# Optimization experiments

Measured on AMD Instinct MI355X. Metric: run time of the kernel, lower is better.

## Reference

```python
import jax, jax.numpy as jnp
import numpy as np

SIGMA = 1.0   # noise std (unit-variance synthetic input)
P = 11        # patch size p1
K = 16        # number of similar patches k1
WIN = 65      # search window w (odd)
S = 3         # reference-patch stride
ALPHA = 0.5   # n2n alpha


def _unfold(x, ksize, stride):
    # (N,1,H,W) -> (N, ksize*ksize, Ho, Wo); kernel positions row-major (== torch F.unfold for C=1)
    return jax.lax.conv_general_dilated_patches(
        x, (ksize, ksize), (stride, stride), 'VALID',
        dimension_numbers=('NCHW', 'OIHW', 'NCHW'))


def block_matching(x, k, p, w, s):
    N, _, H, W = x.shape
    v = w // 2
    assert (H - p + 1) % s == 1 and (W - p + 1) % s == 1  # no edge-case branches needed
    Href = (H - p) // s + 1
    Wref = (W - p) // s + 1
    x_pad = jnp.pad(x, ((0, 0), (0, 0), (v, v), (v, v)))  # zero pad; invalid candidates masked below
    # |patch|^2 / p^2 at every position of the padded image (== F.avg_pool2d(x**2, p))
    sq = jax.lax.reduce_window(x_pad * x_pad, 0.0, jax.lax.add,
                               (1, 1, p, p), (1, 1, 1, 1), 'VALID') / (p * p)
    norms = _unfold(sq, 2 * v + 1, s)                                  # (N,(2v+1)^2,Href,Wref)
    norms = norms.reshape(N, 2 * v + 1, 2 * v + 1, Href, Wref).transpose(0, 3, 4, 1, 2)
    lw = _unfold(x_pad, 2 * v + p, s) / p                              # (N,(2v+p)^2,Href,Wref)
    lw = lw.reshape(N, 2 * v + p, 2 * v + p, Href, Wref).transpose(0, 3, 4, 1, 2)
    G = N * Href * Wref
    lw = lw.reshape(1, G, 2 * v + p, 2 * v + p)
    ref = lw[0, :, v:-v, v:-v][:, None]                                # (G,1,p,p) reference patches
    sp = jax.lax.conv_general_dilated(
        lw, ref, (1, 1), 'VALID',
        dimension_numbers=('NCHW', 'OIHW', 'NCHW'),
        feature_group_count=G)                                         # (1,G,2v+1,2v+1)
    dist = norms.reshape(1, G, 2 * v + 1, 2 * v + 1) - 2.0 * sp
    dist = dist.reshape(N, Href, Wref, 2 * v + 1, 2 * v + 1)
    # mask candidate patches that fall outside the original image (torch uses NaN padding + topk)
    offs = jnp.arange(-v, v + 1)
    hr = jnp.arange(Href) * s
    wr = jnp.arange(Wref) * s
    row_ok = (hr[:, None] + offs >= 0) & (hr[:, None] + offs <= H - p)  # (Href, 2v+1)
    col_ok = (wr[:, None] + offs >= 0) & (wr[:, None] + offs <= W - p)  # (Wref, 2v+1)
    valid = row_ok[:, None, :, None] & col_ok[None, :, None, :]
    dist = jnp.where(valid[None], dist, jnp.inf)
    dist = dist.at[..., v, v].set(-jnp.inf)                            # reference patch always kept
    dist = dist.reshape(N, Href, Wref, (2 * v + 1) ** 2)
    _, idx = jax.lax.top_k(-dist, k)                                   # k smallest distances
    ind_row = idx // (2 * v + 1) - v
    ind_col = idx % (2 * v + 1) - v
    ind = (ind_row + hr[None, :, None, None]) * (W - p + 1) + (ind_col + wr[None, None, :, None])
    return ind.reshape(N, -1)                                          # (N, Href*Wref*k)


def gather_groups(y, indices, k, p):
    N = y.shape[0]
    uf = _unfold(y, p, 1).reshape(N, p * p, -1)                        # (N, n, (H-p+1)(W-p+1))
    Yg = jnp.take_along_axis(uf, indices[:, None, :], axis=2)          # (N, n, L*k)
    L = indices.shape[1] // k
    return Yg.reshape(N, p * p, L, k).transpose(0, 2, 3, 1)            # (N, L, k, n)


def denoise1(Y, sigma):
    # method='n2n', constraints='affine'
    N, B, k, n = Y.shape
    D = n * sigma ** 2
    E = n * ALPHA ** 2 * sigma ** 2
    Ik = jnp.eye(k, dtype=Y.dtype)
    Q = Y @ jnp.swapaxes(Y, 2, 3) + E * Ik                             # (N,B,k,k), SPD
    Lc = jnp.linalg.cholesky(Q)
    Ikb = jnp.broadcast_to(Ik, Q.shape)
    Z = jax.scipy.linalg.solve_triangular(Lc, Ikb, lower=True)
    Qinv = jax.scipy.linalg.solve_triangular(jnp.swapaxes(Lc, 2, 3), Z, lower=False)
    Qinv1 = jnp.sum(Qinv, axis=3, keepdims=True)
    Qinv2 = jnp.sum(Qinv1, axis=2, keepdims=True)
    theta = Ik - (Qinv - (Qinv1 @ jnp.swapaxes(Qinv1, 2, 3)) / Qinv2) * (D + E)
    theta = jnp.swapaxes(theta, 2, 3)
    X_hat = theta @ Y
    weights = 1.0 / jnp.clip(jnp.sum(theta * theta, axis=3, keepdims=True), 1.0 / k, 1.0)
    return X_hat, weights


def _fold(x, H, W, p):
    # inverse of unfold: sum overlapping p x p patches back onto the image grid
    N, n, _ = x.shape
    Hp, Wp = H - p + 1, W - p + 1
    x = x.reshape(N, p, p, Hp, Wp)
    out = jnp.zeros((N, 1, H, W), x.dtype)
    for a in range(p):
        for b in range(p):
            out = out.at[:, 0, a:a + Hp, b:b + Wp].add(x[:, a, b])
    return out


def aggregate(X_hat, weights, indices, H, W, p):
    N, L, k, n = X_hat.shape
    X = (X_hat * weights).reshape(N, L * k, n).transpose(0, 2, 1)      # (N, n, L*k)
    Wt = jnp.broadcast_to(weights, (N, L, k, n)).reshape(N, L * k, n).transpose(0, 2, 1)
    Lfull = (H - p + 1) * (W - p + 1)
    def scat(vals, idx):
        return jnp.zeros((n, Lfull), vals.dtype).at[:, idx].add(vals)
    X_sum = jax.vmap(scat)(X, indices)
    W_sum = jax.vmap(scat)(Wt, indices)
    return _fold(X_sum, H, W, p) / _fold(W_sum, H, W, p)


def _forward(y):
    N, C, H, W = y.shape
    indices = block_matching(y, K, P, WIN, S)
    Yg = gather_groups(y, indices, K, P)
    X_hat, weights = denoise1(Yg, SIGMA)
    return aggregate(X_hat, weights, indices, H, W, P)


def setup_inputs():
    key = jax.random.key(0)
    y = jax.random.normal(key, (4, 1, 128, 128), dtype=jnp.float32)
    return {"y": y}


def reference(y):
    return _forward(y)
```

## Files before the change

kernel.cpp:

```cpp
#include <hip/hip_runtime.h>
#include <math.h>

#define HH 128
#define WW 128
#define NIMG 4
#define PP 11
#define KSIM 16
#define STRIDE_S 3
#define VRAD 32
#define WINW 65
#define NTASK (WINW*9)
#define HREF 40
#define WREF 40
#define NPOS 118
#define WROWS 75
#define WPITCH 84
#define NGROUP (NIMG*HREF*WREF)
#define EPS_E 30.25f
#define DE_C 151.25f
#define INFD 3.0e38f
#define RTASK (VRAD*9 + VRAD/8)

#define FOOT 84
#define FPITCH 85
#define SPITCH 88

__global__ __launch_bounds__(256, 5)
void bm_kernel(const float* __restrict__ y, int* __restrict__ inds)
{
    __shared__ float win[WROWS][WPITCH];
    __shared__ float candv[4][16];
    __shared__ int   candi[4][16];

    const int blk = blockIdx.x;
    const int n   = blk / (HREF*WREF);
    const int rem = blk % (HREF*WREF);
    const int hr  = (rem / WREF) * STRIDE_S;
    const int wr  = (rem % WREF) * STRIDE_S;
    const float* img = y + n * HH * WW;
    const int tid = threadIdx.x;

    for (int t = tid; t < WROWS * WPITCH; t += 256) {
        int r = t / WPITCH, c = t % WPITCH;
        int gr = hr - VRAD + r, gc = wr - VRAD + c;
        float v = 0.f;
        if (c < WROWS && gr >= 0 && gr < HH && gc >= 0 && gc < WW)
            v = img[gr * WW + gc];
        win[r][c] = v;
    }
    __syncthreads();

    float d[3][8];
#pragma unroll
    for (int s = 0; s < 3; s++)
#pragma unroll
        for (int c = 0; c < 8; c++) d[s][c] = INFD;

#pragma unroll
    for (int s = 0; s < 3; s++) {
        int task = tid + (s << 8);
        if (task < NTASK) {
            int drx = task / 9;
            int c0  = (task % 9) * 8;
            int rr  = hr + drx - VRAD;
            bool rowok = (rr >= 0 && rr <= HH - PP);
            if (rowok) {
                float dot[8];
                float colsq[18];
#pragma unroll
                for (int c = 0; c < 8; c++) dot[c] = 0.f;
#pragma unroll
                for (int j2 = 0; j2 < 18; j2++) colsq[j2] = 0.f;
                for (int a = 0; a < PP; a++) {
                    const float4* w4 = reinterpret_cast<const float4*>(&win[drx + a][c0]);
                    float4 A0 = w4[0], A1 = w4[1], A2 = w4[2], A3 = w4[3];
                    float2 A4 = *reinterpret_cast<const float2*>(&win[drx + a][c0 + 16]);
                    float wv[18] = {A0.x,A0.y,A0.z,A0.w, A1.x,A1.y,A1.z,A1.w,
                                    A2.x,A2.y,A2.z,A2.w, A3.x,A3.y,A3.z,A3.w,
                                    A4.x,A4.y};
                    const float4* r4 = reinterpret_cast<const float4*>(&win[VRAD + a][VRAD]);
                    float4 R0 = r4[0], R1 = r4[1];
                    float2 R2 = *reinterpret_cast<const float2*>(&win[VRAD + a][VRAD + 8]);
                    float  R3 = win[VRAD + a][VRAD + 10];
                    float rv[11] = {R0.x,R0.y,R0.z,R0.w, R1.x,R1.y,R1.z,R1.w,
                                    R2.x,R2.y, R3};
#pragma unroll
                    for (int j2 = 0; j2 < 18; j2++) colsq[j2] += wv[j2] * wv[j2];
#pragma unroll
                    for (int b = 0; b < PP; b++) {
#pragma unroll
                        for (int c = 0; c < 8; c++)
                            dot[c] += wv[b + c] * rv[b];
                    }
                }
#pragma unroll
                for (int j2 = 1; j2 < 18; j2++) colsq[j2] += colsq[j2 - 1];
#pragma unroll
                for (int c = 0; c < 8; c++) {
                    int dcx = c0 + c;
                    int cc  = wr + dcx - VRAD;
                    float norm = colsq[c + 10] - (c ? colsq[c - 1] : 0.f);
                    if (dcx < WINW && cc >= 0 && cc <= WW - PP)
                        d[s][c] = norm - 2.f * dot[c];
                }
            }
            if (task == RTASK) d[s][0] = -INFD;
        }
    }

    float lval = INFD; int lidx = 0;
#pragma unroll
    for (int s = 0; s < 3; s++)
#pragma unroll
        for (int c = 0; c < 8; c++)
            if (d[s][c] < lval) { lval = d[s][c]; lidx = (s << 3) | c; }

    const int wvid = tid >> 6, lane = tid & 63;
    for (int sel = 0; sel < KSIM; sel++) {
        float rv = lval;
        int   ri = ((tid + ((lidx >> 3) << 8)) << 3) | (lidx & 7);
#pragma unroll
        for (int off = 32; off > 0; off >>= 1) {
            float ov = __shfl_down(rv, off);
            int   oi = __shfl_down(ri, off);
            if (ov < rv) { rv = ov; ri = oi; }
        }
        if (lane == 0) { candv[wvid][sel] = rv; candi[wvid][sel] = ri; }
        int bi = __shfl(ri, 0);
        int otid = (bi >> 3) & 255;
        if (tid == otid) {
            int code = (((bi >> 3) >> 8) << 3) | (bi & 7);
            lval = INFD; lidx = 0;
#pragma unroll
            for (int s = 0; s < 3; s++)
#pragma unroll
                for (int c = 0; c < 8; c++) {
                    if (((s << 3) | c) == code) d[s][c] = INFD;
                    if (d[s][c] < lval) { lval = d[s][c]; lidx = (s << 3) | c; }
                }
        }
    }
    __syncthreads();

    if (wvid == 0) {
        float v  = candv[lane >> 4][lane & 15];
        int   ci = candi[lane >> 4][lane & 15];
        for (int sel = 0; sel < KSIM; sel++) {
            float rv = v; int ri = ci; int rl = lane;
#pragma unroll
            for (int off = 32; off > 0; off >>= 1) {
                float ov = __shfl_down(rv, off);
                int   oi = __shfl_down(ri, off);
                int   ol = __shfl_down(rl, off);
                if (ov < rv) { rv = ov; ri = oi; rl = ol; }
            }
            int bi = __shfl(ri, 0);
            int bl = __shfl(rl, 0);
            if (lane == 0) {
                int task2 = bi >> 3;
                int drx = task2 / 9, dcx = (task2 % 9) * 8 + (bi & 7);
                inds[blk * KSIM + sel] =
                    (hr + drx - VRAD) * NPOS + (wr + dcx - VRAD);
            }
            if (lane == bl) v = INFD;
        }
    }
}

__global__ __launch_bounds__(512, 1)
void dn_kernel(const float* __restrict__ y, const int* __restrict__ inds,
               float2* __restrict__ nd, int R)
{
    __shared__ float  src[FOOT][SPITCH];
    __shared__ float2 acc[FOOT][FPITCH];
    __shared__ float  Qm[16][16][17];
    __shared__ float  s1[16][16];
    __shared__ float  s2[16];
    __shared__ float  wl[16][16];
    __shared__ short  pr_[16][16], pc_[16][16];

    const int blk = blockIdx.x;
    const int n  = blk / 100;
    const int tr = blk % 100;
    const int ti = tr / 10, tj = tr % 10;
    const int r0 = 12*ti - VRAD, c0 = 12*tj - VRAD;
    const int tid = threadIdx.x;
    const float* img = y + n * HH * WW;

    if (tid < 256) {
        int g = tid >> 4, m = tid & 15;
        int gg = n*(HREF*WREF) + (ti*4 + (g >> 2))*WREF + (tj*4 + (g & 3));
        int idx = inds[gg*KSIM + m];
        pr_[g][m] = (short)(idx / NPOS);
        pc_[g][m] = (short)(idx % NPOS);
    }
    for (int t = tid; t < FOOT*FOOT; t += 512) {
        int rr = t / FOOT, cc = t % FOOT;
        int gr = r0 + rr, gc = c0 + cc;
        float v = 0.f;
        if (gr >= 0 && gr < HH && gc >= 0 && gc < WW) v = img[gr*WW + gc];
        src[rr][cc] = v;
    }
    for (int t = tid; t < FOOT*FPITCH; t += 512)
        acc[t/FPITCH][t%FPITCH] = make_float2(0.f, 0.f);
    __syncthreads();

    for (int k = 0; k < 5; k++) {
        int task = tid + k*512;
        if (task < 16*136) {
            int g = task / 136, e = task % 136;
            int i = (int)((sqrtf(8.f*(float)e + 1.f) - 1.f) * 0.5f + 1e-4f);
            int j = e - i*(i+1)/2;
            int ari = pr_[g][i] - r0, aci = pc_[g][i] - c0;
            int arj = pr_[g][j] - r0, acj = pc_[g][j] - c0;
            float s = (i == j) ? EPS_E : 0.f;
            for (int a = 0; a < PP; a++) {
                const float* Ri = &src[ari + a][aci];
                const float* Rj = &src[arj + a][acj];
#pragma unroll
                for (int b = 0; b < PP; b++) s += Ri[b] * Rj[b];
            }
            Qm[g][i][j] = s;
            Qm[g][j][i] = s;
        }
    }
    __syncthreads();

    const int uu = tid >> 8, ii = (tid >> 4) & 15, jj = tid & 15;
    for (int ks = 0; ks < 16; ks++) {
        float fA[8], rk[8], pv[8], aij[8];
#pragma unroll
        for (int k = 0; k < 8; k++) {
            int g = uu + 2*k;
            fA[k]  = Qm[g][ii][ks];
            rk[k]  = Qm[g][ks][jj];
            pv[k]  = Qm[g][ks][ks];
            aij[k] = Qm[g][ii][jj];
        }
        __syncthreads();
#pragma unroll
        for (int k = 0; k < 8; k++) {
            int g = uu + 2*k;
            float inv = 1.f / pv[k];
            float nv;
            if (ii == ks) nv = (jj == ks) ? inv : rk[k] * inv;
            else          nv = (jj == ks) ? -fA[k] * inv : aij[k] - fA[k] * rk[k] * inv;
            Qm[g][ii][jj] = nv;
        }
        __syncthreads();
    }

    if (tid < 256) {
        int g = tid >> 4, a = tid & 15;
        float s = 0.f;
#pragma unroll
        for (int b = 0; b < 16; b++) s += Qm[g][a][b];
        s1[g][a] = s;
    }
    __syncthreads();
    if (tid < 16) {
        float s = 0.f;
#pragma unroll
        for (int a = 0; a < 16; a++) s += s1[tid][a];
        s2[tid] = s;
    }
    __syncthreads();
#pragma unroll
    for (int k = 0; k < 8; k++) {
        int g = uu + 2*k;
        float t = ((ii == jj) ? 1.f : 0.f)
                - (Qm[g][ii][jj] - s1[g][ii]*s1[g][jj]/s2[g]) * DE_C;
        Qm[g][ii][jj] = t;
    }
    __syncthreads();
    if (tid < 256) {
        int g = tid >> 4, r = tid & 15;
        float s = 0.f;
#pragma unroll
        for (int m2 = 0; m2 < 16; m2++) { float t = Qm[g][m2][r]; s += t*t; }
        s = fminf(fmaxf(s, 1.f/16.f), 1.f);
        wl[g][r] = 1.f / s;
    }
    __syncthreads();

    for (int it = 0; it < 2; it++) {
        int task = tid + it*512;
        if (task < 16*61) {
            int g = task / 61, s = task % 61;
            int pxa = 2*s;
            bool okB = (pxa + 1 < 121);
            int dra = pxa / 11, dca = pxa % 11;
            int drb = dra, dcb = dca + 1;
            if (dcb == 11) { drb = dra + 1; dcb = 0; }
            if (!okB) { drb = dra; dcb = dca; }

            int baseS[16];
#pragma unroll
            for (int m = 0; m < 16; m++)
                baseS[m] = ((int)pr_[g][m] - r0) * SPITCH + ((int)pc_[g][m] - c0);

            const float* sf = &src[0][0];
            float xhA[16], xhB[16];
#pragma unroll
            for (int r = 0; r < 16; r++) { xhA[r] = 0.f; xhB[r] = 0.f; }
            const int offA = dra*SPITCH + dca, offB = drb*SPITCH + dcb;
#pragma unroll
            for (int m = 0; m < 16; m++) {
                float yvA = sf[baseS[m] + offA];
                float yvB = sf[baseS[m] + offB];
#pragma unroll
                for (int r = 0; r < 16; r++) {
                    float t = Qm[g][m][r];
                    xhA[r] += t * yvA;
                    xhB[r] += t * yvB;
                }
            }
#pragma unroll
            for (int r = 0; r < 16; r++) {
                float wv2 = wl[g][r];
                int ar = (int)pr_[g][r] - r0, ac = (int)pc_[g][r] - c0;
                float* cA = (float*)&acc[ar + dra][ac + dca];
                __hip_atomic_fetch_add(cA,     wv2 * xhA[r],
                    __ATOMIC_RELAXED, __HIP_MEMORY_SCOPE_WORKGROUP);
                __hip_atomic_fetch_add(cA + 1, wv2,
                    __ATOMIC_RELAXED, __HIP_MEMORY_SCOPE_WORKGROUP);
                if (okB) {
                    float* cB = (float*)&acc[ar + drb][ac + dcb];
                    __hip_atomic_fetch_add(cB,     wv2 * xhB[r],
                        __ATOMIC_RELAXED, __HIP_MEMORY_SCOPE_WORKGROUP);
                    __hip_atomic_fetch_add(cB + 1, wv2,
                        __ATOMIC_RELAXED, __HIP_MEMORY_SCOPE_WORKGROUP);
                }
            }
        }
    }
    __syncthreads();

    float2* ndI = nd + ((size_t)(blk & (R - 1)) * NIMG + n) * HH * WW;
    for (int t = tid; t < FOOT * FOOT; t += 512) {
        int rr = t / FOOT, cc = t % FOOT;
        float2 v = acc[rr][cc];
        if (v.y != 0.f) {
            int px = (r0 + rr) * WW + (c0 + cc);
#if defined(__has_builtin) && __has_builtin(__builtin_amdgcn_global_atomic_fadd_v2f32)
            typedef float v2f __attribute__((ext_vector_type(2)));
            __builtin_amdgcn_global_atomic_fadd_v2f32((v2f*)&ndI[px], (v2f){v.x, v.y});
#else
            atomicAdd(&ndI[px].x, v.x);
            atomicAdd(&ndI[px].y, v.y);
#endif
        }
    }
}

__global__ __launch_bounds__(256)
void fin_kernel(const float2* __restrict__ nd, float* __restrict__ out, int R)
{
    int t = blockIdx.x * 256 + threadIdx.x;
    if (t < NIMG * HH * WW) {
        float sn = 0.f, sd = 0.f;
        for (int r = 0; r < R; r++) {
            float2 v = nd[(size_t)r * NIMG * HH * WW + t];
            sn += v.x; sd += v.y;
        }
        out[t] = sn / sd;
    }
}

extern "C" void kernel_launch(void* const* d_in, const int* in_sizes, int n_in,
                              void* d_out, int out_size, void* d_ws, size_t ws_size,
                              hipStream_t stream)
{
    const float* y = (const float*)d_in[0];
    float* out = (float*)d_out;

    size_t indsBytes = (size_t)NGROUP * KSIM * sizeof(int);
    size_t perRep    = (size_t)NIMG * HH * WW * sizeof(float2);
    int R = 1;
    while (R < 4 && indsBytes + perRep * (size_t)(R * 2) <= ws_size) R <<= 1;

    float2* nd  = (float2*)d_ws;
    int*    inds = (int*)((char*)d_ws + perRep * (size_t)R);

    hipMemsetAsync(nd, 0, perRep * (size_t)R, stream);
    bm_kernel<<<NGROUP, 256, 0, stream>>>(y, inds);
    dn_kernel<<<NIMG * 100, 512, 0, stream>>>(y, inds, nd, R);
    fin_kernel<<<(NIMG * HH * WW + 255) / 256, 256, 0, stream>>>(nd, out, R);
}
```

Measured before the change: 504.3 us.

## Tile block matching over 4x4 reference groups with shared row-dot reuse

Block matching moves from one workgroup per reference patch to one workgroup per 4x4 tile of reference patches. Each tile computes 11-wide row dot products in shared memory once, and those partial sums are reused across the overlapping references. Patch norms are precomputed by a new kernel, and each reference keeps a per-lane sorted top-16 list, merged across 16 lanes with xor shuffles. The denoise kernel's shared accumulator is split into two halves to cut LDS use and raise occupancy, at the cost of a second pass with extra syncs.

```diff
diff --git a/kernel.cpp b/kernel.cpp
--- a/kernel.cpp
+++ b/kernel.cpp
@@ -9,170 +9,173 @@
 #define STRIDE_S 3
 #define VRAD 32
 #define WINW 65
-#define NTASK (WINW*9)
 #define HREF 40
 #define WREF 40
 #define NPOS 118
-#define WROWS 75
-#define WPITCH 84
 #define NGROUP (NIMG*HREF*WREF)
 #define EPS_E 30.25f
 #define DE_C 151.25f
 #define INFD 3.0e38f
-#define RTASK (VRAD*9 + VRAD/8)
 
 #define FOOT 84
 #define FPITCH 85
 #define SPITCH 88
-
-__global__ __launch_bounds__(256, 5)
-void bm_kernel(const float* __restrict__ y, int* __restrict__ inds)
+#define IPITCH 100
+#define PD2 388
+#define DBATCH 96
+#define PADW 72
+#define PADDD (WINW*PADW)
+#define NBATCH 49
+#define CNP 120
+
+__global__ __launch_bounds__(128)
+void bm_norm(const float* __restrict__ y, float* __restrict__ cnorm)
 {
-    __shared__ float win[WROWS][WPITCH];
-    __shared__ float candv[4][16];
-    __shared__ int   candi[4][16];
+    int n = blockIdx.x / NPOS, rr = blockIdx.x % NPOS;
+    int cc = threadIdx.x;
+    if (cc < NPOS) {
+        const float* img = y + n * HH * WW;
+        float s = 0.f;
+        for (int a = 0; a < PP; a++) {
+            const float* rp = &img[(rr + a) * WW + cc];
+#pragma unroll
+            for (int b = 0; b < PP; b++) s += rp[b] * rp[b];
+        }
+        cnorm[n * NPOS * CNP + rr * CNP + cc] = s;
+    }
+}
+
+__global__ __launch_bounds__(256, 2)
+void bm_kernel(const float* __restrict__ y, const float* __restrict__ cnorm,
+               int* __restrict__ inds)
+{
+    __shared__ float timg[FOOT][IPITCH];
+    __shared__ float D2[20][PD2];
 
     const int blk = blockIdx.x;
-    const int n   = blk / (HREF*WREF);
-    const int rem = blk % (HREF*WREF);
-    const int hr  = (rem / WREF) * STRIDE_S;
-    const int wr  = (rem % WREF) * STRIDE_S;
+    const int n  = blk / 100;
+    const int tr = blk % 100;
+    const int ti = tr / 10, tj = tr % 10;
+    const int r0 = 12 * ti - VRAD, c0 = 12 * tj - VRAD;
+    const int tid = threadIdx.x;
     const float* img = y + n * HH * WW;
-    const int tid = threadIdx.x;
-
-    for (int t = tid; t < WROWS * WPITCH; t += 256) {
-        int r = t / WPITCH, c = t % WPITCH;
-        int gr = hr - VRAD + r, gc = wr - VRAD + c;
+    const float* cn  = cnorm + n * NPOS * CNP;
+
+    for (int t = tid; t < FOOT * IPITCH; t += 256) {
+        int r = t / IPITCH, c = t % IPITCH;
+        int gr = r0 + r, gc = c0 + c;
         float v = 0.f;
-        if (c < WROWS && gr >= 0 && gr < HH && gc >= 0 && gc < WW)
+        if (c < FOOT && gr >= 0 && gr < HH && gc >= 0 && gc < WW)
             v = img[gr * WW + gc];
-        win[r][c] = v;
-    }
-    __syncthreads();
-
-    float d[3][8];
-#pragma unroll
-    for (int s = 0; s < 3; s++)
-#pragma unroll
-        for (int c = 0; c < 8; c++) d[s][c] = INFD;
-
-#pragma unroll
-    for (int s = 0; s < 3; s++) {
-        int task = tid + (s << 8);
-        if (task < NTASK) {
-            int drx = task / 9;
-            int c0  = (task % 9) * 8;
-            int rr  = hr + drx - VRAD;
-            bool rowok = (rr >= 0 && rr <= HH - PP);
-            if (rowok) {
-                float dot[8];
-                float colsq[18];
-#pragma unroll
-                for (int c = 0; c < 8; c++) dot[c] = 0.f;
-#pragma unroll
-                for (int j2 = 0; j2 < 18; j2++) colsq[j2] = 0.f;
-                for (int a = 0; a < PP; a++) {
-                    const float4* w4 = reinterpret_cast<const float4*>(&win[drx + a][c0]);
-                    float4 A0 = w4[0], A1 = w4[1], A2 = w4[2], A3 = w4[3];
-                    float2 A4 = *reinterpret_cast<const float2*>(&win[drx + a][c0 + 16]);
-                    float wv[18] = {A0.x,A0.y,A0.z,A0.w, A1.x,A1.y,A1.z,A1.w,
-                                    A2.x,A2.y,A2.z,A2.w, A3.x,A3.y,A3.z,A3.w,
-                                    A4.x,A4.y};
-                    const float4* r4 = reinterpret_cast<const float4*>(&win[VRAD + a][VRAD]);
-                    float4 R0 = r4[0], R1 = r4[1];
-                    float2 R2 = *reinterpret_cast<const float2*>(&win[VRAD + a][VRAD + 8]);
-                    float  R3 = win[VRAD + a][VRAD + 10];
-                    float rv[11] = {R0.x,R0.y,R0.z,R0.w, R1.x,R1.y,R1.z,R1.w,
-                                    R2.x,R2.y, R3};
-#pragma unroll
-                    for (int j2 = 0; j2 < 18; j2++) colsq[j2] += wv[j2] * wv[j2];
-#pragma unroll
-                    for (int b = 0; b < PP; b++) {
-#pragma unroll
-                        for (int c = 0; c < 8; c++)
-                            dot[c] += wv[b + c] * rv[b];
+        timg[r][c] = v;
+    }
+    __syncthreads();
+
+    float sv[16]; int si[16];
+#pragma unroll
+    for (int q = 0; q < 16; q++) { sv[q] = INFD; si[q] = 0; }
+
+    const int prow1 = tid / 12;
+    const int dcc   = tid % 12;
+    const int refq  = tid >> 4;
+    const int dl    = tid & 15;
+    const int u = refq >> 2, v = refq & 3;
+    const int hr = 3 * (4 * ti + u), wr = 3 * (4 * tj + v);
+
+#pragma unroll 1
+    for (int b = 0; b < NBATCH; b++) {
+        if (tid < 240) {
+            int ddp0 = b * DBATCH + dcc * 8;
+            if (ddp0 < PADDD) {
+                int dr   = ddp0 / PADW - VRAD;
+                int dcx0 = ddp0 % PADW;
+                const float* row1 = &timg[(VRAD + prow1)][VRAD];
+                const float* row2 = &timg[(VRAD + prow1 + dr)][dcx0];
+                float a1[20], a2[27];
+#pragma unroll
+                for (int q = 0; q < 5; q++) {
+                    float4 x4 = ((const float4*)row1)[q];
+                    a1[4*q] = x4.x; a1[4*q+1] = x4.y; a1[4*q+2] = x4.z; a1[4*q+3] = x4.w;
+                }
+#pragma unroll
+                for (int q = 0; q < 27; q++) a2[q] = row2[q];
+#pragma unroll
+                for (int k = 0; k < 8; k++) {
+                    float d0 = 0.f, d1 = 0.f, d2 = 0.f, d3 = 0.f;
+#pragma unroll
+                    for (int bb = 0; bb < PP; bb++) {
+                        d0 += a1[bb]     * a2[bb + k];
+                        d1 += a1[3 + bb] * a2[3 + bb + k];
+                        d2 += a1[6 + bb] * a2[6 + bb + k];
+                        d3 += a1[9 + bb] * a2[9 + bb + k];
+                    }
+                    *(float4*)&D2[prow1][(dcc * 8 + k) * 4] = make_float4(d0, d1, d2, d3);
+                }
+            }
+        }
+        __syncthreads();
+#pragma unroll
+        for (int kk = 0; kk < 6; kk++) {
+            int d = dl + 16 * kk;
+            int ddp = b * DBATCH + d;
+            if (ddp < PADDD) {
+                int dcx = ddp % PADW;
+                if (dcx < WINW) {
+                    int dr = ddp / PADW - VRAD, dc = dcx - VRAD;
+                    int rr = hr + dr, cc = wr + dc;
+                    if (rr >= 0 && rr <= HH - PP && cc >= 0 && cc <= WW - PP) {
+                        float dot = 0.f;
+#pragma unroll
+                        for (int a = 0; a < PP; a++)
+                            dot += D2[3 * u + a][d * 4 + v];
+                        float val = cn[rr * CNP + cc] - 2.f * dot;
+                        if (dr == 0 && dc == 0) val = -INFD;
+                        if (val < sv[15]) {
+                            sv[15] = val; si[15] = ddp;
+#pragma unroll
+                            for (int q = 15; q > 0; q--) {
+                                if (sv[q] < sv[q - 1]) {
+                                    float tv = sv[q]; sv[q] = sv[q-1]; sv[q-1] = tv;
+                                    int   tq = si[q]; si[q] = si[q-1]; si[q-1] = tq;
+                                }
+                            }
+                        }
                     }
                 }
-#pragma unroll
-                for (int j2 = 1; j2 < 18; j2++) colsq[j2] += colsq[j2 - 1];
-#pragma unroll
-                for (int c = 0; c < 8; c++) {
-                    int dcx = c0 + c;
-                    int cc  = wr + dcx - VRAD;
-                    float norm = colsq[c + 10] - (c ? colsq[c - 1] : 0.f);
-                    if (dcx < WINW && cc >= 0 && cc <= WW - PP)
-                        d[s][c] = norm - 2.f * dot[c];
-                }
             }
-            if (task == RTASK) d[s][0] = -INFD;
-        }
-    }
-
-    float lval = INFD; int lidx = 0;
-#pragma unroll
-    for (int s = 0; s < 3; s++)
-#pragma unroll
-        for (int c = 0; c < 8; c++)
-            if (d[s][c] < lval) { lval = d[s][c]; lidx = (s << 3) | c; }
-
-    const int wvid = tid >> 6, lane = tid & 63;
+        }
+        __syncthreads();
+    }
+
+    const int gref = n * (HREF * WREF) + (ti * 4 + u) * WREF + (tj * 4 + v);
+#pragma unroll 1
     for (int sel = 0; sel < KSIM; sel++) {
-        float rv = lval;
-        int   ri = ((tid + ((lidx >> 3) << 8)) << 3) | (lidx & 7);
-#pragma unroll
-        for (int off = 32; off > 0; off >>= 1) {
-            float ov = __shfl_down(rv, off);
-            int   oi = __shfl_down(ri, off);
-            if (ov < rv) { rv = ov; ri = oi; }
-        }
-        if (lane == 0) { candv[wvid][sel] = rv; candi[wvid][sel] = ri; }
-        int bi = __shfl(ri, 0);
-        int otid = (bi >> 3) & 255;
-        if (tid == otid) {
-            int code = (((bi >> 3) >> 8) << 3) | (bi & 7);
-            lval = INFD; lidx = 0;
-#pragma unroll
-            for (int s = 0; s < 3; s++)
-#pragma unroll
-                for (int c = 0; c < 8; c++) {
-                    if (((s << 3) | c) == code) d[s][c] = INFD;
-                    if (d[s][c] < lval) { lval = d[s][c]; lidx = (s << 3) | c; }
-                }
-        }
-    }
-    __syncthreads();
-
-    if (wvid == 0) {
-        float v  = candv[lane >> 4][lane & 15];
-        int   ci = candi[lane >> 4][lane & 15];
-        for (int sel = 0; sel < KSIM; sel++) {
-            float rv = v; int ri = ci; int rl = lane;
-#pragma unroll
-            for (int off = 32; off > 0; off >>= 1) {
-                float ov = __shfl_down(rv, off);
-                int   oi = __shfl_down(ri, off);
-                int   ol = __shfl_down(rl, off);
-                if (ov < rv) { rv = ov; ri = oi; rl = ol; }
-            }
-            int bi = __shfl(ri, 0);
-            int bl = __shfl(rl, 0);
-            if (lane == 0) {
-                int task2 = bi >> 3;
-                int drx = task2 / 9, dcx = (task2 % 9) * 8 + (bi & 7);
-                inds[blk * KSIM + sel] =
-                    (hr + drx - VRAD) * NPOS + (wr + dcx - VRAD);
-            }
-            if (lane == bl) v = INFD;
+        float bv = sv[0]; int bi = si[0]; int bl = dl;
+#pragma unroll
+        for (int m = 1; m < 16; m <<= 1) {
+            float ov = __shfl_xor(bv, m, 16);
+            int   oi = __shfl_xor(bi, m, 16);
+            int   ol = __shfl_xor(bl, m, 16);
+            if (ov < bv || (ov == bv && ol < bl)) { bv = ov; bi = oi; bl = ol; }
+        }
+        if (dl == 0) {
+            int dr = bi / PADW - VRAD, dc = bi % PADW - VRAD;
+            inds[gref * KSIM + sel] = (hr + dr) * NPOS + (wr + dc);
+        }
+        if (dl == bl) {
+#pragma unroll
+            for (int q = 0; q < 15; q++) { sv[q] = sv[q + 1]; si[q] = si[q + 1]; }
+            sv[15] = INFD;
         }
     }
 }
 
-__global__ __launch_bounds__(512, 1)
+__global__ __launch_bounds__(512, 4)
 void dn_kernel(const float* __restrict__ y, const int* __restrict__ inds,
                float2* __restrict__ nd, int R)
 {
     __shared__ float  src[FOOT][SPITCH];
-    __shared__ float2 acc[FOOT][FPITCH];
+    __shared__ float2 accH[42][FPITCH];
     __shared__ float  Qm[16][16][17];
     __shared__ float  s1[16][16];
     __shared__ float  s2[16];
@@ -183,34 +186,32 @@
     const int n  = blk / 100;
     const int tr = blk % 100;
     const int ti = tr / 10, tj = tr % 10;
-    const int r0 = 12*ti - VRAD, c0 = 12*tj - VRAD;
+    const int r0 = 12 * ti - VRAD, c0 = 12 * tj - VRAD;
     const int tid = threadIdx.x;
     const float* img = y + n * HH * WW;
 
     if (tid < 256) {
         int g = tid >> 4, m = tid & 15;
-        int gg = n*(HREF*WREF) + (ti*4 + (g >> 2))*WREF + (tj*4 + (g & 3));
-        int idx = inds[gg*KSIM + m];
+        int gg = n * (HREF * WREF) + (ti * 4 + (g >> 2)) * WREF + (tj * 4 + (g & 3));
+        int idx = inds[gg * KSIM + m];
         pr_[g][m] = (short)(idx / NPOS);
         pc_[g][m] = (short)(idx % NPOS);
     }
-    for (int t = tid; t < FOOT*FOOT; t += 512) {
+    for (int t = tid; t < FOOT * FOOT; t += 512) {
         int rr = t / FOOT, cc = t % FOOT;
         int gr = r0 + rr, gc = c0 + cc;
-        float v = 0.f;
-        if (gr >= 0 && gr < HH && gc >= 0 && gc < WW) v = img[gr*WW + gc];
-        src[rr][cc] = v;
-    }
-    for (int t = tid; t < FOOT*FPITCH; t += 512)
-        acc[t/FPITCH][t%FPITCH] = make_float2(0.f, 0.f);
+        float vv = 0.f;
+        if (gr >= 0 && gr < HH && gc >= 0 && gc < WW) vv = img[gr * WW + gc];
+        src[rr][cc] = vv;
+    }
     __syncthreads();
 
     for (int k = 0; k < 5; k++) {
-        int task = tid + k*512;
-        if (task < 16*136) {
+        int task = tid + k * 512;
+        if (task < 16 * 136) {
             int g = task / 136, e = task % 136;
-            int i = (int)((sqrtf(8.f*(float)e + 1.f) - 1.f) * 0.5f + 1e-4f);
-            int j = e - i*(i+1)/2;
+            int i = (int)((sqrtf(8.f * (float)e + 1.f) - 1.f) * 0.5f + 1e-4f);
+            int j = e - i * (i + 1) / 2;
             int ari = pr_[g][i] - r0, aci = pc_[g][i] - c0;
             int arj = pr_[g][j] - r0, acj = pc_[g][j] - c0;
             float s = (i == j) ? EPS_E : 0.f;
@@ -231,7 +232,7 @@
         float fA[8], rk[8], pv[8], aij[8];
 #pragma unroll
         for (int k = 0; k < 8; k++) {
-            int g = uu + 2*k;
+            int g = uu + 2 * k;
             fA[k]  = Qm[g][ii][ks];
             rk[k]  = Qm[g][ks][jj];
             pv[k]  = Qm[g][ks][ks];
@@ -240,7 +241,7 @@
         __syncthreads();
 #pragma unroll
         for (int k = 0; k < 8; k++) {
-            int g = uu + 2*k;
+            int g = uu + 2 * k;
             float inv = 1.f / pv[k];
             float nv;
             if (ii == ks) nv = (jj == ks) ? inv : rk[k] * inv;
@@ -254,7 +255,7 @@
         int g = tid >> 4, a = tid & 15;
         float s = 0.f;
 #pragma unroll
-        for (int b = 0; b < 16; b++) s += Qm[g][a][b];
+        for (int b2 = 0; b2 < 16; b2++) s += Qm[g][a][b2];
         s1[g][a] = s;
     }
     __syncthreads();
@@ -267,9 +268,9 @@
     __syncthreads();
 #pragma unroll
     for (int k = 0; k < 8; k++) {
-        int g = uu + 2*k;
+        int g = uu + 2 * k;
         float t = ((ii == jj) ? 1.f : 0.f)
-                - (Qm[g][ii][jj] - s1[g][ii]*s1[g][jj]/s2[g]) * DE_C;
+                - (Qm[g][ii][jj] - s1[g][ii] * s1[g][jj] / s2[g]) * DE_C;
         Qm[g][ii][jj] = t;
     }
     __syncthreads();
@@ -277,79 +278,92 @@
         int g = tid >> 4, r = tid & 15;
         float s = 0.f;
 #pragma unroll
-        for (int m2 = 0; m2 < 16; m2++) { float t = Qm[g][m2][r]; s += t*t; }
-        s = fminf(fmaxf(s, 1.f/16.f), 1.f);
+        for (int m2 = 0; m2 < 16; m2++) { float t = Qm[g][m2][r]; s += t * t; }
+        s = fminf(fmaxf(s, 1.f / 16.f), 1.f);
         wl[g][r] = 1.f / s;
     }
     __syncthreads();
 
-    for (int it = 0; it < 2; it++) {
-        int task = tid + it*512;
-        if (task < 16*61) {
-            int g = task / 61, s = task % 61;
-            int pxa = 2*s;
-            bool okB = (pxa + 1 < 121);
-            int dra = pxa / 11, dca = pxa % 11;
-            int drb = dra, dcb = dca + 1;
-            if (dcb == 11) { drb = dra + 1; dcb = 0; }
-            if (!okB) { drb = dra; dcb = dca; }
-
-            int baseS[16];
-#pragma unroll
-            for (int m = 0; m < 16; m++)
-                baseS[m] = ((int)pr_[g][m] - r0) * SPITCH + ((int)pc_[g][m] - c0);
-
-            const float* sf = &src[0][0];
-            float xhA[16], xhB[16];
-#pragma unroll
-            for (int r = 0; r < 16; r++) { xhA[r] = 0.f; xhB[r] = 0.f; }
-            const int offA = dra*SPITCH + dca, offB = drb*SPITCH + dcb;
-#pragma unroll
-            for (int m = 0; m < 16; m++) {
-                float yvA = sf[baseS[m] + offA];
-                float yvB = sf[baseS[m] + offB];
+    float2* ndI = nd + ((size_t)(blk & (R - 1)) * NIMG + n) * HH * WW;
+#pragma unroll 1
+    for (int half = 0; half < 2; half++) {
+        const int h0 = half * 42;
+        for (int t = tid; t < 42 * FPITCH; t += 512)
+            accH[t / FPITCH][t % FPITCH] = make_float2(0.f, 0.f);
+        __syncthreads();
+
+        for (int it = 0; it < 2; it++) {
+            int task = tid + it * 512;
+            if (task < 16 * 61) {
+                int g = task / 61, s = task % 61;
+                int pxa = 2 * s;
+                bool okB = (pxa + 1 < 121);
+                int dra = pxa / 11, dca = pxa % 11;
+                int drb = dra, dcb = dca + 1;
+                if (dcb == 11) { drb = dra + 1; dcb = 0; }
+                if (!okB) { drb = dra; dcb = dca; }
+
+                int baseS[16];
+#pragma unroll
+                for (int m = 0; m < 16; m++)
+                    baseS[m] = ((int)pr_[g][m] - r0) * SPITCH + ((int)pc_[g][m] - c0);
+
+                const float* sf = &src[0][0];
+                float xhA[16], xhB[16];
+#pragma unroll
+                for (int r = 0; r < 16; r++) { xhA[r] = 0.f; xhB[r] = 0.f; }
+                const int offA = dra * SPITCH + dca, offB = drb * SPITCH + dcb;
+#pragma unroll
+                for (int m = 0; m < 16; m++) {
+                    float yvA = sf[baseS[m] + offA];
+                    float yvB = sf[baseS[m] + offB];
+#pragma unroll
+                    for (int r = 0; r < 16; r++) {
+                        float t = Qm[g][m][r];
+                        xhA[r] += t * yvA;
+                        xhB[r] += t * yvB;
+                    }
+                }
 #pragma unroll
                 for (int r = 0; r < 16; r++) {
-                    float t = Qm[g][m][r];
-                    xhA[r] += t * yvA;
-                    xhB[r] += t * yvB;
+                    float wv2 = wl[g][r];
+                    int ar = (int)pr_[g][r] - r0, ac = (int)pc_[g][r] - c0;
+                    int hA = ar + dra;
+                    if (hA >= h0 && hA < h0 + 42) {
+                        float* cA = (float*)&accH[hA - h0][ac + dca];
+                        __hip_atomic_fetch_add(cA,     wv2 * xhA[r],
+                            __ATOMIC_RELAXED, __HIP_MEMORY_SCOPE_WORKGROUP);
+                        __hip_atomic_fetch_add(cA + 1, wv2,
+                            __ATOMIC_RELAXED, __HIP_MEMORY_SCOPE_WORKGROUP);
+                    }
+                    int hB = ar + drb;
+                    if (okB && hB >= h0 && hB < h0 + 42) {
+                        float* cB = (float*)&accH[hB - h0][ac + dcb];
+                        __hip_atomic_fetch_add(cB,     wv2 * xhB[r],
+                            __ATOMIC_RELAXED, __HIP_MEMORY_SCOPE_WORKGROUP);
+                        __hip_atomic_fetch_add(cB + 1, wv2,
+                            __ATOMIC_RELAXED, __HIP_MEMORY_SCOPE_WORKGROUP);
+                    }
                 }
             }
-#pragma unroll
-            for (int r = 0; r < 16; r++) {
-                float wv2 = wl[g][r];
-                int ar = (int)pr_[g][r] - r0, ac = (int)pc_[g][r] - c0;
-                float* cA = (float*)&acc[ar + dra][ac + dca];
-                __hip_atomic_fetch_add(cA,     wv2 * xhA[r],
-                    __ATOMIC_RELAXED, __HIP_MEMORY_SCOPE_WORKGROUP);
-                __hip_atomic_fetch_add(cA + 1, wv2,
-                    __ATOMIC_RELAXED, __HIP_MEMORY_SCOPE_WORKGROUP);
-                if (okB) {
-                    float* cB = (float*)&acc[ar + drb][ac + dcb];
-                    __hip_atomic_fetch_add(cB,     wv2 * xhB[r],
-                        __ATOMIC_RELAXED, __HIP_MEMORY_SCOPE_WORKGROUP);
-                    __hip_atomic_fetch_add(cB + 1, wv2,
-                        __ATOMIC_RELAXED, __HIP_MEMORY_SCOPE_WORKGROUP);
-                }
+        }
+        __syncthreads();
+
+        for (int t = tid; t < 42 * FOOT; t += 512) {
+            int rr = t / FOOT, cc = t % FOOT;
+            float2 vv = accH[rr][cc];
+            if (vv.y != 0.f) {
+                int px = (r0 + h0 + rr) * WW + (c0 + cc);
+#if defined(__has_builtin) && __has_builtin(__builtin_amdgcn_global_atomic_fadd_v2f32)
+                typedef float v2f __attribute__((ext_vector_type(2)));
+                __builtin_amdgcn_global_atomic_fadd_v2f32((v2f*)&ndI[px], (v2f){vv.x, vv.y});
+#else
+                atomicAdd(&ndI[px].x, vv.x);
+                atomicAdd(&ndI[px].y, vv.y);
+#endif
             }
         }
-    }
-    __syncthreads();
-
-    float2* ndI = nd + ((size_t)(blk & (R - 1)) * NIMG + n) * HH * WW;
-    for (int t = tid; t < FOOT * FOOT; t += 512) {
-        int rr = t / FOOT, cc = t % FOOT;
-        float2 v = acc[rr][cc];
-        if (v.y != 0.f) {
-            int px = (r0 + rr) * WW + (c0 + cc);
-#if defined(__has_builtin) && __has_builtin(__builtin_amdgcn_global_atomic_fadd_v2f32)
-            typedef float v2f __attribute__((ext_vector_type(2)));
-            __builtin_amdgcn_global_atomic_fadd_v2f32((v2f*)&ndI[px], (v2f){v.x, v.y});
-#else
-            atomicAdd(&ndI[px].x, v.x);
-            atomicAdd(&ndI[px].y, v.y);
-#endif
-        }
+        __syncthreads();
     }
 }
 
@@ -360,8 +374,8 @@
     if (t < NIMG * HH * WW) {
         float sn = 0.f, sd = 0.f;
         for (int r = 0; r < R; r++) {
-            float2 v = nd[(size_t)r * NIMG * HH * WW + t];
-            sn += v.x; sd += v.y;
+            float2 vv = nd[(size_t)r * NIMG * HH * WW + t];
+            sn += vv.x; sd += vv.y;
         }
         out[t] = sn / sd;
     }
@@ -374,16 +388,19 @@
     const float* y = (const float*)d_in[0];
     float* out = (float*)d_out;
 
-    size_t indsBytes = (size_t)NGROUP * KSIM * sizeof(int);
-    size_t perRep    = (size_t)NIMG * HH * WW * sizeof(float2);
+    size_t perRep = (size_t)NIMG * HH * WW * sizeof(float2);
+    size_t indsB  = (size_t)NGROUP * KSIM * sizeof(int);
+    size_t cnormB = (size_t)NIMG * NPOS * CNP * sizeof(float);
     int R = 1;
-    while (R < 4 && indsBytes + perRep * (size_t)(R * 2) <= ws_size) R <<= 1;
-
-    float2* nd  = (float2*)d_ws;
-    int*    inds = (int*)((char*)d_ws + perRep * (size_t)R);
+    while (R < 4 && perRep * (size_t)(R * 2) + indsB + cnormB <= ws_size) R <<= 1;
+
+    float2* nd    = (float2*)d_ws;
+    int*    inds  = (int*)((char*)d_ws + perRep * (size_t)R);
+    float*  cnorm = (float*)((char*)inds + indsB);
 
     hipMemsetAsync(nd, 0, perRep * (size_t)R, stream);
-    bm_kernel<<<NGROUP, 256, 0, stream>>>(y, inds);
+    bm_norm<<<NIMG * NPOS, 128, 0, stream>>>(y, cnorm);
+    bm_kernel<<<NIMG * 100, 256, 0, stream>>>(y, cnorm, inds);
     dn_kernel<<<NIMG * 100, 512, 0, stream>>>(y, inds, nd, R);
     fin_kernel<<<(NIMG * HH * WW + 255) / 256, 256, 0, stream>>>(nd, out, R);
 }
```

Result: slower. 701.8 us (+39.1%).
